# Performance work log

Hardware: AMD Instinct MI355X
Metric: run time of the kernel (lower is better)

The kernel has to match this reference:

```python
import jax, jax.numpy as jnp
import numpy as np

NUM_HEADS = 12
EMBED_DIM = 768
HEAD_DIM = EMBED_DIM // NUM_HEADS


def _rope_cos_sin():
    # Faithful to source: RoPE is applied with seq_dim=1 on [b,h,n,d] tensors,
    # so the "position" axis is actually the HEAD axis (length NUM_HEADS).
    inv_freq = 1.0 / (10000.0 ** (jnp.arange(0, HEAD_DIM, 2, dtype=jnp.float32) / HEAD_DIM))
    t = jnp.arange(NUM_HEADS, dtype=jnp.float32)
    freqs = t[:, None] * inv_freq[None, :]            # [H, D/2]
    emb = jnp.concatenate([freqs, freqs], axis=-1)     # [H, D]
    cos = jnp.cos(emb)[None, :, None, :]               # [1, H, 1, D] broadcasts over seq
    sin = jnp.sin(emb)[None, :, None, :]
    return cos, sin


def _apply_rope(x, cos, sin):
    # x: [B, H, N, D]
    x1, x2 = jnp.split(x, 2, axis=-1)
    x_rot = jnp.concatenate([-x2, x1], axis=-1)
    return x * cos + x_rot * sin


def setup_inputs() -> dict:
    key = jax.random.key(0)
    k1, k2, k3, k4, k5 = jax.random.split(key, 5)
    B, N, E = 8, 1024, EMBED_DIM
    s_in = 1.0 / np.sqrt(E)
    return {
        "x": jax.random.normal(k1, (B, N, E), dtype=jnp.float32),
        "w_qkv": jax.random.uniform(k2, (E, 3 * E), dtype=jnp.float32, minval=-s_in, maxval=s_in),
        "b_qkv": jax.random.uniform(k3, (3 * E,), dtype=jnp.float32, minval=-s_in, maxval=s_in),
        "w_proj": jax.random.uniform(k4, (E, E), dtype=jnp.float32, minval=-s_in, maxval=s_in),
        "b_proj": jax.random.uniform(k5, (E,), dtype=jnp.float32, minval=-s_in, maxval=s_in),
    }


def reference(x, w_qkv, b_qkv, w_proj, b_proj):
    B, N, E = x.shape
    H, D = NUM_HEADS, HEAD_DIM
    scale = D ** (-0.5)

    qkv = x @ w_qkv + b_qkv                                  # [B, N, 3E]
    qkv = qkv.reshape(B, N, 3, H, D).transpose(2, 0, 3, 1, 4)  # [3, B, H, N, D]
    q, k, v = qkv[0], qkv[1], qkv[2]

    cos, sin = _rope_cos_sin()
    q = _apply_rope(q, cos, sin)
    k = _apply_rope(k, cos, sin)

    attn = jnp.einsum('bhid,bhjd->bhij', q, k) * scale       # [B, H, N, N]
    attn = jax.nn.softmax(attn, axis=-1)
    out = jnp.einsum('bhij,bhjd->bhid', attn, v)             # [B, H, N, D]
    out = out.transpose(0, 2, 1, 3).reshape(B, N, E)         # [B, N, E]
    return out @ w_proj + b_proj
```

## Files before the change

kernel.cpp:

```cpp
#include <hip/hip_runtime.h>
#include <math.h>

#define NH 12
#define HD 64
#define NSEQ 1024
#define BATCH 8
#define EMB 768
#define NQKV 2304
#define MROWS 8192

typedef _Float16 half8 __attribute__((ext_vector_type(8)));
typedef _Float16 half4 __attribute__((ext_vector_type(4)));
typedef _Float16 half2v __attribute__((ext_vector_type(2)));
typedef float f32x4 __attribute__((ext_vector_type(4)));
typedef float f32x16 __attribute__((ext_vector_type(16)));
typedef unsigned int u32;

#define MFMA16(a,b,c) __builtin_amdgcn_mfma_f32_16x16x32_f16(a, b, c, 0, 0, 0)
#define MFMA32(a,b,c) __builtin_amdgcn_mfma_f32_32x32x16_f16(a, b, c, 0, 0, 0)

__device__ __forceinline__ void gld_lds16(const _Float16* g, _Float16* l) {
  __builtin_amdgcn_global_load_lds((const __attribute__((address_space(1))) u32*)g,
                                   (__attribute__((address_space(3))) u32*)l, 16, 0, 0);
}

__global__ __launch_bounds__(256) void cvt_f16(const float* __restrict__ in,
                                               _Float16* __restrict__ out, int n4) {
  int i = blockIdx.x * 256 + threadIdx.x;
  if (i < n4) {
    float4 v = ((const float4*)in)[i];
    half4 h = { (_Float16)v.x, (_Float16)v.y, (_Float16)v.z, (_Float16)v.w };
    ((half4*)out)[i] = h;
  }
}

__global__ __launch_bounds__(256) void transpose_cvt(const float* __restrict__ in,
                                                     _Float16* __restrict__ out,
                                                     int R, int C) {
  __shared__ _Float16 T[64][72];
  const int tr = blockIdx.y * 64, tc = blockIdx.x * 64;
  const int r = threadIdx.x >> 2, s = threadIdx.x & 3;
  const float* src = in + (size_t)(tr + r) * C + tc + s * 16;
  _Float16* dst = &T[r][s * 16];
  #pragma unroll
  for (int i = 0; i < 4; ++i) {
    float4 v = ((const float4*)src)[i];
    dst[4*i+0] = (_Float16)v.x; dst[4*i+1] = (_Float16)v.y;
    dst[4*i+2] = (_Float16)v.z; dst[4*i+3] = (_Float16)v.w;
  }
  __syncthreads();
  alignas(16) _Float16 tmp[16];
  #pragma unroll
  for (int j = 0; j < 16; ++j) tmp[j] = T[s * 16 + j][r];
  half8* o = (half8*)(out + (size_t)(tc + r) * R + tr + s * 16);
  o[0] = *(half8*)&tmp[0];
  o[1] = *(half8*)&tmp[8];
}

template<int MODE>
__global__ __launch_bounds__(256) void gemm_mfma(const _Float16* __restrict__ A,
                                                 const _Float16* __restrict__ BT,
                                                 const float* __restrict__ bias,
                                                 float* __restrict__ outf,
                                                 _Float16* __restrict__ qo,
                                                 _Float16* __restrict__ ko,
                                                 _Float16* __restrict__ vo,
                                                 int K) {
  const int BUFH = 128 * 32;
  __shared__ __align__(16) _Float16 As[2 * 128 * 32];
  __shared__ __align__(16) _Float16 Bs[2 * 128 * 32];
  const int tid = threadIdx.x;
  const int lane = tid & 63, wave = tid >> 6;
  const int quad = lane >> 4, l15 = lane & 15;
  const int wm = (wave >> 1) * 64, wn = (wave & 1) * 64;
  const int row0 = blockIdx.y * 128, col0 = blockIdx.x * 128;

  const int srow = lane >> 2, sseg = lane & 3;
  const _Float16* gA = A + (size_t)(row0 + wave*32 + srow) * K + sseg * 8;
  const _Float16* gB = BT + (size_t)(col0 + wave*32 + srow) * K + sseg * 8;
  _Float16* lA0 = As + (wave*32) * 32;
  _Float16* lA1 = As + (wave*32 + 16) * 32;
  _Float16* lB0 = Bs + (wave*32) * 32;
  _Float16* lB1 = Bs + (wave*32 + 16) * 32;

  f32x4 acc[4][4];
  #pragma unroll
  for (int i = 0; i < 4; ++i)
    #pragma unroll
    for (int j = 0; j < 4; ++j) {
      f32x4 z = {0.f, 0.f, 0.f, 0.f};
      acc[i][j] = z;
    }

  gld_lds16(gA,          lA0);
  gld_lds16(gA + 16 * K, lA1);
  gld_lds16(gB,          lB0);
  gld_lds16(gB + 16 * K, lB1);

  int buf = 0;
  for (int k0 = 0; k0 < K; k0 += 32, buf ^= 1) {
    __syncthreads();
    if (k0 + 32 < K) {
      const int nb = (buf ^ 1) * BUFH;
      gld_lds16(gA + k0 + 32,          lA0 + nb);
      gld_lds16(gA + k0 + 32 + 16 * K, lA1 + nb);
      gld_lds16(gB + k0 + 32,          lB0 + nb);
      gld_lds16(gB + k0 + 32 + 16 * K, lB1 + nb);
    }
    const _Float16* Ab = As + buf * BUFH;
    const _Float16* Bb = Bs + buf * BUFH;
    half8 af[4], bf[4];
    #pragma unroll
    for (int mt = 0; mt < 4; ++mt)
      af[mt] = *(const half8*)(Ab + (wm + mt*16 + l15) * 32 + quad * 8);
    #pragma unroll
    for (int nt = 0; nt < 4; ++nt)
      bf[nt] = *(const half8*)(Bb + (wn + nt*16 + l15) * 32 + quad * 8);
    #pragma unroll
    for (int mt = 0; mt < 4; ++mt)
      #pragma unroll
      for (int nt = 0; nt < 4; ++nt)
        acc[mt][nt] = MFMA16(af[mt], bf[nt], acc[mt][nt]);
  }

  float bcol[4];
  #pragma unroll
  for (int nt = 0; nt < 4; ++nt)
    bcol[nt] = bias[col0 + wn + nt*16 + l15];

  if (MODE == 0) {
    const int ch = col0 + wn;
    const int tt = ch / EMB;
    const int hh = (ch % EMB) >> 6;
    float cs[2], sn[2];
    if (tt < 2) {
      #pragma unroll
      for (int j = 0; j < 2; ++j) {
        float fi = (float)(j*16 + l15);
        float ang = (float)hh * expf(-0.28782313662425574f * fi);
        sincosf(ang, &sn[j], &cs[j]);
      }
    }
    #pragma unroll
    for (int mt = 0; mt < 4; ++mt) {
      int m0 = row0 + wm + mt*16 + quad*4;
      int b = m0 >> 10, n0 = m0 & 1023;
      size_t bh = (size_t)(b * NH + hh);
      if (tt == 2) {
        #pragma unroll
        for (int nt = 0; nt < 4; ++nt) {
          int d = nt*16 + l15;
          half4 pk;
          #pragma unroll
          for (int r = 0; r < 4; ++r)
            pk[r] = (_Float16)(acc[mt][nt][r] + bcol[nt]);
          *(half4*)(vo + (bh * HD + d) * NSEQ + n0) = pk;
        }
      } else {
        _Float16* dst = (tt == 0) ? qo : ko;
        const float sc = (tt == 0) ? 0.125f : 1.0f;
        #pragma unroll
        for (int j = 0; j < 2; ++j) {
          #pragma unroll
          for (int r = 0; r < 4; ++r) {
            float lo = acc[mt][j][r]     + bcol[j];
            float hi = acc[mt][j + 2][r] + bcol[j + 2];
            float nlo = (lo * cs[j] - hi * sn[j]) * sc;
            float nhi = (hi * cs[j] + lo * sn[j]) * sc;
            size_t rowoff = (bh * NSEQ + (size_t)(n0 + r)) * HD;
            dst[rowoff + j*16 + l15]      = (_Float16)nlo;
            dst[rowoff + j*16 + l15 + 32] = (_Float16)nhi;
          }
        }
      }
    }
  } else {
    #pragma unroll
    for (int mt = 0; mt < 4; ++mt) {
      int m0 = row0 + wm + mt*16 + quad*4;
      #pragma unroll
      for (int nt = 0; nt < 4; ++nt)
        #pragma unroll
        for (int r = 0; r < 4; ++r)
          outf[(size_t)(m0 + r) * EMB + col0 + wn + nt*16 + l15] =
              acc[mt][nt][r] + bcol[nt];
    }
  }
}

__global__ __launch_bounds__(256) void attn_mfma32(const _Float16* __restrict__ q,
                                                   const _Float16* __restrict__ k,
                                                   const _Float16* __restrict__ vt,
                                                   _Float16* __restrict__ ao) {
  const int BUFH = 64 * 64;
  __shared__ __align__(16) _Float16 Ks[2 * 64 * 64];
  __shared__ __align__(16) _Float16 Vs[2 * 64 * 64];
  const int tid = threadIdx.x;
  const int lane = tid & 63, wave = tid >> 6;
  const int l31 = lane & 31, hi = lane >> 5;
  const int bh = blockIdx.y;
  const int qrow = blockIdx.x * 128 + wave * 32 + l31;
  const size_t base = (size_t)bh * NSEQ * HD;

  const _Float16* qp = q + base + (size_t)qrow * HD + hi * 8;
  half8 qf[4];
  #pragma unroll
  for (int kh = 0; kh < 4; ++kh)
    qf[kh] = *(const half8*)(qp + kh * 16);

  const int srow = lane >> 3;
  const int sxor = (lane & 7) ^ (srow & 7);
  const _Float16* kg = k + base + (size_t)(wave*16 + srow) * HD + sxor * 8;
  const _Float16* vg = vt + (size_t)bh * HD * NSEQ
                       + (size_t)(wave*16 + srow) * NSEQ + sxor * 8;
  const int lofs = (wave * 16) * 64;

  int xofs[4];
  #pragma unroll
  for (int kh = 0; kh < 4; ++kh)
    xofs[kh] = ((kh*2 + hi) ^ (l31 & 7)) * 8;

  f32x16 O[2];
  #pragma unroll
  for (int dt = 0; dt < 2; ++dt)
    #pragma unroll
    for (int r = 0; r < 16; ++r) O[dt][r] = 0.f;
  float l = 0.f;

  gld_lds16(kg,             Ks + lofs);
  gld_lds16(kg + 8 * HD,    Ks + lofs + 8 * 64);
  gld_lds16(vg,             Vs + lofs);
  gld_lds16(vg + 8 * NSEQ,  Vs + lofs + 8 * 64);

  int buf = 0;
  for (int c0 = 0; c0 < NSEQ; c0 += 64, buf ^= 1) {
    __syncthreads();
    if (c0 + 64 < NSEQ) {
      const int nb = (buf ^ 1) * BUFH;
      gld_lds16(kg + (size_t)(c0 + 64) * HD,      Ks + nb + lofs);
      gld_lds16(kg + (size_t)(c0 + 72) * HD,      Ks + nb + lofs + 8 * 64);
      gld_lds16(vg + c0 + 64,                     Vs + nb + lofs);
      gld_lds16(vg + 8 * NSEQ + c0 + 64,          Vs + nb + lofs + 8 * 64);
    }
    const _Float16* Kb = Ks + buf * BUFH;
    const _Float16* Vb = Vs + buf * BUFH;

    f32x16 ct[2];
    #pragma unroll
    for (int kt = 0; kt < 2; ++kt) {
      #pragma unroll
      for (int r = 0; r < 16; ++r) ct[kt][r] = 0.f;
      #pragma unroll
      for (int kh = 0; kh < 4; ++kh) {
        half8 kf = *(const half8*)(Kb + (kt*32 + l31) * 64 + xofs[kh]);
        ct[kt] = MFMA32(kf, qf[kh], ct[kt]);
      }
    }

    union { half2v v; int i; } ph2[16];
    float rs = 0.f;
    #pragma unroll
    for (int kt = 0; kt < 2; ++kt)
      #pragma unroll
      for (int rp = 0; rp < 8; ++rp) {
        float p0 = __expf(ct[kt][2*rp]     - 4.0f);
        float p1 = __expf(ct[kt][2*rp + 1] - 4.0f);
        rs += p0 + p1;
        half2v hp = { (_Float16)p0, (_Float16)p1 };
        ph2[kt*8 + rp].v = hp;
      }
    l += rs;

    #pragma unroll
    for (int kh = 0; kh < 4; ++kh) {
      const int kt = kh >> 1;
      const int iA = kt*8 + 4*(kh & 1);
      int a0 = ph2[iA].i,     a1 = ph2[iA + 1].i;
      int b0 = ph2[iA + 2].i, b1 = ph2[iA + 3].i;
      int own0 = hi ? b0 : a0, own1 = hi ? b1 : a1;
      int snd0 = hi ? a0 : b0, snd1 = hi ? a1 : b1;
      int r0 = __shfl_xor(snd0, 32), r1 = __shfl_xor(snd1, 32);
      union { half8 h; int d[4]; } pf;
      pf.d[0] = hi ? r0 : own0;  pf.d[1] = hi ? r1 : own1;
      pf.d[2] = hi ? own0 : r0;  pf.d[3] = hi ? own1 : r1;
      #pragma unroll
      for (int dt = 0; dt < 2; ++dt) {
        half8 vf = *(const half8*)(Vb + (dt*32 + l31) * 64 + xofs[kh]);
        O[dt] = MFMA32(vf, pf.h, O[dt]);
      }
    }
  }

  l += __shfl_xor(l, 32);

  const int b = bh / NH, hh = bh % NH;
  const float inv = 1.0f / l;
  _Float16* orow = ao + (size_t)(b * NSEQ + qrow) * EMB + hh * HD;
  #pragma unroll
  for (int dt = 0; dt < 2; ++dt)
    #pragma unroll
    for (int t = 0; t < 4; ++t) {
      int d0 = dt*32 + 8*t + 4*hi;
      half4 o4;
      #pragma unroll
      for (int j = 0; j < 4; ++j)
        o4[j] = (_Float16)(O[dt][4*t + j] * inv);
      *(half4*)(orow + d0) = o4;
    }
}

extern "C" void kernel_launch(void* const* d_in, const int* in_sizes, int n_in,
                              void* d_out, int out_size, void* d_ws, size_t ws_size,
                              hipStream_t stream) {
  const float* x      = (const float*)d_in[0];
  const float* w_qkv  = (const float*)d_in[1];
  const float* b_qkv  = (const float*)d_in[2];
  const float* w_proj = (const float*)d_in[3];
  const float* b_proj = (const float*)d_in[4];
  float* out = (float*)d_out;

  _Float16* xh  = (_Float16*)d_ws;
  _Float16* wqT = xh  + (size_t)MROWS * EMB;
  _Float16* wpT = wqT + (size_t)NQKV * EMB;
  _Float16* qh  = wpT + (size_t)EMB * EMB;
  _Float16* kh  = qh  + (size_t)BATCH*NH*NSEQ*HD;
  _Float16* vth = kh  + (size_t)BATCH*NH*NSEQ*HD;
  _Float16* aoh = vth + (size_t)BATCH*NH*NSEQ*HD;

  cvt_f16<<<(MROWS*EMB/4 + 255)/256, 256, 0, stream>>>(x, xh, MROWS*EMB/4);
  transpose_cvt<<<dim3(NQKV/64, EMB/64), 256, 0, stream>>>(w_qkv, wqT, EMB, NQKV);
  transpose_cvt<<<dim3(EMB/64, EMB/64), 256, 0, stream>>>(w_proj, wpT, EMB, EMB);

  gemm_mfma<0><<<dim3(NQKV/128, MROWS/128), 256, 0, stream>>>(
      xh, wqT, b_qkv, nullptr, qh, kh, vth, EMB);

  attn_mfma32<<<dim3(NSEQ/128, BATCH*NH), 256, 0, stream>>>(qh, kh, vth, aoh);

  gemm_mfma<1><<<dim3(EMB/128, MROWS/128), 256, 0, stream>>>(
      aoh, wpT, b_proj, out, nullptr, nullptr, nullptr, EMB);
}
```

Measured before the change: 213.0 us.

## Merge prepass kernels, swizzle GEMM LDS tiles, and permute V to drop shuffles

Merges the x conversion and the two weight-transpose kernels into one launch that dispatches on block index. It applies an XOR swizzle to the GEMM LDS tile layout, on both the global-to-LDS load and the fragment reads, to reduce bank conflicts. It also writes V with a permuted sequence index so the attention P·V step can use the softmax registers directly, removing the cross-half wave shuffles. The V permutation must match the attention kernel's V read offsets exactly, or the result is wrong.

New measurement: 205.7 us. 3.4% less time.

```diff
diff --git a/kernel.cpp b/kernel.cpp
--- a/kernel.cpp
+++ b/kernel.cpp
@@ -24,21 +24,11 @@
                                    (__attribute__((address_space(3))) u32*)l, 16, 0, 0);
 }
 
-__global__ __launch_bounds__(256) void cvt_f16(const float* __restrict__ in,
-                                               _Float16* __restrict__ out, int n4) {
-  int i = blockIdx.x * 256 + threadIdx.x;
-  if (i < n4) {
-    float4 v = ((const float4*)in)[i];
-    half4 h = { (_Float16)v.x, (_Float16)v.y, (_Float16)v.z, (_Float16)v.w };
-    ((half4*)out)[i] = h;
-  }
-}
-
-__global__ __launch_bounds__(256) void transpose_cvt(const float* __restrict__ in,
-                                                     _Float16* __restrict__ out,
-                                                     int R, int C) {
-  __shared__ _Float16 T[64][72];
-  const int tr = blockIdx.y * 64, tc = blockIdx.x * 64;
+__device__ __forceinline__ void transpose_tile(const float* __restrict__ in,
+                                               _Float16* __restrict__ out,
+                                               int R, int C, int bx, int by,
+                                               _Float16 (*T)[72]) {
+  const int tr = by * 64, tc = bx * 64;
   const int r = threadIdx.x >> 2, s = threadIdx.x & 3;
   const float* src = in + (size_t)(tr + r) * C + tc + s * 16;
   _Float16* dst = &T[r][s * 16];
@@ -55,6 +45,28 @@
   half8* o = (half8*)(out + (size_t)(tc + r) * R + tr + s * 16);
   o[0] = *(half8*)&tmp[0];
   o[1] = *(half8*)&tmp[8];
+}
+
+__global__ __launch_bounds__(256) void prepass(const float* __restrict__ x,
+                                               _Float16* __restrict__ xh,
+                                               const float* __restrict__ wq,
+                                               _Float16* __restrict__ wqT,
+                                               const float* __restrict__ wp,
+                                               _Float16* __restrict__ wpT) {
+  __shared__ _Float16 T[64][72];
+  const int bid = blockIdx.x;
+  if (bid < 6144) {
+    int i = bid * 256 + threadIdx.x;
+    float4 v = ((const float4*)x)[i];
+    half4 h = { (_Float16)v.x, (_Float16)v.y, (_Float16)v.z, (_Float16)v.w };
+    ((half4*)xh)[i] = h;
+  } else if (bid < 6576) {
+    int idx = bid - 6144;
+    transpose_tile(wq, wqT, EMB, NQKV, idx % 36, idx / 36, T);
+  } else {
+    int idx = bid - 6576;
+    transpose_tile(wp, wpT, EMB, EMB, idx % 12, idx / 12, T);
+  }
 }
 
 template<int MODE>
@@ -75,13 +87,16 @@
   const int wm = (wave >> 1) * 64, wn = (wave & 1) * 64;
   const int row0 = blockIdx.y * 128, col0 = blockIdx.x * 128;
 
-  const int srow = lane >> 2, sseg = lane & 3;
+  const int srow = lane >> 2;
+  const int sseg = (lane & 3) ^ ((srow >> 1) & 3);
   const _Float16* gA = A + (size_t)(row0 + wave*32 + srow) * K + sseg * 8;
   const _Float16* gB = BT + (size_t)(col0 + wave*32 + srow) * K + sseg * 8;
   _Float16* lA0 = As + (wave*32) * 32;
   _Float16* lA1 = As + (wave*32 + 16) * 32;
   _Float16* lB0 = Bs + (wave*32) * 32;
   _Float16* lB1 = Bs + (wave*32 + 16) * 32;
+
+  const int xq = (quad ^ ((l15 >> 1) & 3)) * 8;
 
   f32x4 acc[4][4];
   #pragma unroll
@@ -112,10 +127,10 @@
     half8 af[4], bf[4];
     #pragma unroll
     for (int mt = 0; mt < 4; ++mt)
-      af[mt] = *(const half8*)(Ab + (wm + mt*16 + l15) * 32 + quad * 8);
+      af[mt] = *(const half8*)(Ab + (wm + mt*16 + l15) * 32 + xq);
     #pragma unroll
     for (int nt = 0; nt < 4; ++nt)
-      bf[nt] = *(const half8*)(Bb + (wn + nt*16 + l15) * 32 + quad * 8);
+      bf[nt] = *(const half8*)(Bb + (wn + nt*16 + l15) * 32 + xq);
     #pragma unroll
     for (int mt = 0; mt < 4; ++mt)
       #pragma unroll
@@ -147,6 +162,7 @@
       int b = m0 >> 10, n0 = m0 & 1023;
       size_t bh = (size_t)(b * NH + hh);
       if (tt == 2) {
+        int np = (n0 & ~12) | ((n0 & 4) << 1) | ((n0 & 8) >> 1);
         #pragma unroll
         for (int nt = 0; nt < 4; ++nt) {
           int d = nt*16 + l15;
@@ -154,7 +170,7 @@
           #pragma unroll
           for (int r = 0; r < 4; ++r)
             pk[r] = (_Float16)(acc[mt][nt][r] + bcol[nt]);
-          *(half4*)(vo + (bh * HD + d) * NSEQ + n0) = pk;
+          *(half4*)(vo + (bh * HD + d) * NSEQ + np) = pk;
         }
       } else {
         _Float16* dst = (tt == 0) ? qo : ko;
@@ -274,15 +290,10 @@
     #pragma unroll
     for (int kh = 0; kh < 4; ++kh) {
       const int kt = kh >> 1;
-      const int iA = kt*8 + 4*(kh & 1);
-      int a0 = ph2[iA].i,     a1 = ph2[iA + 1].i;
-      int b0 = ph2[iA + 2].i, b1 = ph2[iA + 3].i;
-      int own0 = hi ? b0 : a0, own1 = hi ? b1 : a1;
-      int snd0 = hi ? a0 : b0, snd1 = hi ? a1 : b1;
-      int r0 = __shfl_xor(snd0, 32), r1 = __shfl_xor(snd1, 32);
+      const int iA = kt*8 + (kh & 1)*4;
       union { half8 h; int d[4]; } pf;
-      pf.d[0] = hi ? r0 : own0;  pf.d[1] = hi ? r1 : own1;
-      pf.d[2] = hi ? own0 : r0;  pf.d[3] = hi ? own1 : r1;
+      pf.d[0] = ph2[iA].i;     pf.d[1] = ph2[iA + 1].i;
+      pf.d[2] = ph2[iA + 2].i; pf.d[3] = ph2[iA + 3].i;
       #pragma unroll
       for (int dt = 0; dt < 2; ++dt) {
         half8 vf = *(const half8*)(Vb + (dt*32 + l31) * 64 + xofs[kh]);
@@ -327,9 +338,7 @@
   _Float16* vth = kh  + (size_t)BATCH*NH*NSEQ*HD;
   _Float16* aoh = vth + (size_t)BATCH*NH*NSEQ*HD;
 
-  cvt_f16<<<(MROWS*EMB/4 + 255)/256, 256, 0, stream>>>(x, xh, MROWS*EMB/4);
-  transpose_cvt<<<dim3(NQKV/64, EMB/64), 256, 0, stream>>>(w_qkv, wqT, EMB, NQKV);
-  transpose_cvt<<<dim3(EMB/64, EMB/64), 256, 0, stream>>>(w_proj, wpT, EMB, EMB);
+  prepass<<<6720, 256, 0, stream>>>(x, xh, w_qkv, wqT, w_proj, wpT);
 
   gemm_mfma<0><<<dim3(NQKV/128, MROWS/128), 256, 0, stream>>>(
       xh, wqT, b_qkv, nullptr, qh, kh, vth, EMB);
```
